# Kernel optimization log

Hardware: AMD Instinct MI355X
Metric: run time of the kernel (lower is better)

Reference implementation:

```python
import jax, jax.numpy as jnp
import numpy as np

BATCH = 32
NUM_VARS = 16
SAMPLES = 4096
EMBED_DIM = 128
WINDOW_SIZE = 32
STEP_SIZE = 4
WIDTH = 1.0


def setup_inputs() -> dict:
    key = jax.random.key(0)
    k1, k2, k3, k4, k5 = jax.random.split(key, 5)
    x = jax.random.normal(k1, (BATCH, NUM_VARS, SAMPLES), dtype=jnp.float32)
    # sample-level LSH: num_variables -> embed_dim
    W_sample = jax.random.normal(k2, (NUM_VARS, EMBED_DIM), dtype=jnp.float32)
    b_sample = jax.random.uniform(k3, (EMBED_DIM,), dtype=jnp.float32, minval=0.0, maxval=WIDTH)
    # patch-level LSH: window_size*embed_dim -> embed_dim
    W_patch = jax.random.normal(k4, (WINDOW_SIZE * EMBED_DIM, EMBED_DIM), dtype=jnp.float32)
    b_patch = jax.random.uniform(k5, (EMBED_DIM,), dtype=jnp.float32, minval=0.0, maxval=WIDTH)
    return {"x": x, "W_sample": W_sample, "b_sample": b_sample,
            "W_patch": W_patch, "b_patch": b_patch}


def reference(x, W_sample, b_sample, W_patch, b_patch):
    batch, v, samples = x.shape
    # encode: E2LSH hash of every timestep, fully vectorized over the samples axis
    # enc: [B, S, D]
    enc = jnp.floor((jnp.einsum('bvs,vd->bsd', x, W_sample) + b_sample) / WIDTH)
    # quantize: sliding windows over time, flattened then hashed
    num_tokens = (samples - WINDOW_SIZE) // STEP_SIZE  # matches preallocated tokens
    # idx: [T, W] gather indices for all windows at once
    idx = jnp.arange(num_tokens)[:, None] * STEP_SIZE + jnp.arange(WINDOW_SIZE)[None, :]
    windows = enc[:, idx, :].reshape(batch, num_tokens, WINDOW_SIZE * EMBED_DIM)  # [B, T, W*D]
    tokens = jnp.floor((windows @ W_patch + b_patch) / WIDTH)  # [B, T, D]
    return tokens
```

## Files before the change

### kernel.cpp

```cpp
#include <hip/hip_runtime.h>
#include <hip/hip_bf16.h>
#include <cstdint>

#define BATCH   32
#define NVARS   16
#define SAMPLES 4096
#define EDIM    128
#define NTOK    1016
#define PLELEM  4368

typedef __bf16 bf8_t __attribute__((ext_vector_type(8)));
typedef float  f4_t  __attribute__((ext_vector_type(4)));

__global__ __launch_bounds__(256) void prep_kernel(
    const float* __restrict__ Wp, __hip_bfloat16* __restrict__ WtF)
{
  __shared__ float ls[32][132];
  int tid = threadIdx.x;
  int kb  = blockIdx.x;
  int s = kb >> 3, dlt = kb & 7;
  int kbase = (4 * dlt + (s & 3)) * 128 + (s >> 2) * 32;
#pragma unroll
  for (int r = 0; r < 16; ++r) {
    int idx = tid + r * 256;
    ls[idx >> 7][idx & 127] =
        Wp[(size_t)(kbase + (idx >> 7)) * EDIM + (idx & 127)];
  }
  __syncthreads();
  int g = tid >> 5, l5 = tid & 31;
#pragma unroll
  for (int h = 0; h < 2; ++h) {
    int lane = l5 + h * 32;
    int quad = lane >> 4, l15 = lane & 15;
    int n = g * 16 + l15;
    union { unsigned short u[8]; uint4 v; } pk;
#pragma unroll
    for (int t = 0; t < 8; ++t) {
      __hip_bfloat16 hh = __float2bfloat16(ls[quad * 8 + t][n]);
      pk.u[t] = *(unsigned short*)&hh;
    }
    *(uint4*)(WtF + (size_t)kb * 4096 + g * 512 + lane * 8) = pk.v;
  }
}

__global__ __launch_bounds__(512, 1) void fused_kernel(
    const float* __restrict__ x,
    const float* __restrict__ Ws,
    const float* __restrict__ bs,
    const __hip_bfloat16* __restrict__ WtF,
    const float* __restrict__ bp,
    float* __restrict__ out)
{
  __shared__ __align__(16) __hip_bfloat16 Apan[16 * PLELEM];
  __shared__ __align__(16) float xTp[2][136][16];

  int tid  = threadIdx.x;
  int lane = tid & 63;
  int wv   = tid >> 6;
  int g    = wv >> 2;
  int wq   = wv & 3;
  int b    = blockIdx.x >> 3;
  int t0   = (blockIdx.x & 7) << 7;
  int wm   = (wq >> 1) << 6;
  int wn   = (wq & 1) << 6;
  int quad = lane >> 4;
  int l15  = lane & 15;

  const __hip_bfloat16* bg = WtF + (size_t)(wn >> 4) * 512 + lane * 8;

  int q4 = tid & 31;
  int eq = q4 >> 3;
  int cq = (q4 >> 1) & 3;
  int hq = q4 & 1;
  int r0 = tid >> 5;

  float w[NVARS][4];
  float bz[4];
  {
    int d0 = q4 * 4;
#pragma unroll
    for (int v = 0; v < NVARS; ++v)
      *(float4*)&w[v][0] = *(const float4*)(Ws + v * EDIM + d0);
    *(float4*)&bz[0] = *(const float4*)(bs + d0);
  }

  int vv = tid & 15, rr = tid >> 4;
  float4 xreg[5];
  {
    const float* xb = x + ((size_t)b * NVARS + vv) * SAMPLES;
#pragma unroll
    for (int j = 0; j < 4; ++j) {
      int s4 = (t0 + rr + 32 * j) * 4;
      xreg[j] = *(const float4*)(xb + s4);
    }
    if (tid < 128) {
      int s4 = (t0 + 128 + rr) * 4;
      if (s4 > SAMPLES - 4) s4 = SAMPLES - 4;
      xreg[4] = *(const float4*)(xb + s4);
    }
  }

  auto stageX = [&](int p, int buf) {
#pragma unroll
    for (int j = 0; j < 4; ++j) {
      float c = (p == 0) ? xreg[j].x : (p == 1) ? xreg[j].y
              : (p == 2) ? xreg[j].z : xreg[j].w;
      xTp[buf][rr + 32 * j][vv] = c;
    }
    if (tid < 128) {
      float c = (p == 0) ? xreg[4].x : (p == 1) ? xreg[4].y
              : (p == 2) ? xreg[4].z : xreg[4].w;
      xTp[buf][128 + rr][vv] = c;
    }
  };

  auto encTask = [&](int p, int buf, int r) {
    const float* xr = &xTp[buf][r][0];
    float xv[NVARS];
    *(float4*)&xv[0]  = *(const float4*)(xr + 0);
    *(float4*)&xv[4]  = *(const float4*)(xr + 4);
    *(float4*)&xv[8]  = *(const float4*)(xr + 8);
    *(float4*)&xv[12] = *(const float4*)(xr + 12);
    float a0 = bz[0], a1 = bz[1], a2 = bz[2], a3 = bz[3];
#pragma unroll
    for (int v = 0; v < NVARS; ++v) {
      a0 += xv[v] * w[v][0]; a1 += xv[v] * w[v][1];
      a2 += xv[v] * w[v][2]; a3 += xv[v] * w[v][3];
    }
    union { unsigned short us[4]; uint2 q; } pk;
    pk.us[0] = (unsigned short)(__float_as_uint(floorf(a0)) >> 16);
    pk.us[1] = (unsigned short)(__float_as_uint(floorf(a1)) >> 16);
    pk.us[2] = (unsigned short)(__float_as_uint(floorf(a2)) >> 16);
    pk.us[3] = (unsigned short)(__float_as_uint(floorf(a3)) >> 16);
    int phys = (cq + (r >> 1)) & 3;
    char* plbase = (char*)&Apan[(eq * 4 + p) * PLELEM];
    *(uint2*)(plbase + r * 64 + phys * 16 + hq * 8) = pk.q;
  };

  stageX(0, 0);
  __syncthreads();
#pragma unroll
  for (int p = 0; p < 4; ++p) {
    if (p < 3) stageX(p + 1, (p + 1) & 1);
    int buf = p & 1;
#pragma unroll
    for (int j = 0; j < 8; ++j) encTask(p, buf, r0 + 16 * j);
    if (tid < 256) encTask(p, buf, 128 + (tid >> 5));
    __syncthreads();
  }

  f4_t acc[4][4];
  f4_t zero = {0.f, 0.f, 0.f, 0.f};
#pragma unroll
  for (int i = 0; i < 4; ++i)
#pragma unroll
    for (int j = 0; j < 4; ++j) acc[i][j] = zero;

  auto loadB = [&](int kb, uint4* d) {
#pragma unroll
    for (int j = 0; j < 4; ++j)
      d[j] = *(const uint4*)(bg + (size_t)kb * 4096 + j * 512);
  };

  auto compute = [&](const bf8_t* pA, int dlt, const uint4* bq_) {
    int swzA = (quad + ((t0 + dlt + wm + l15) >> 1)) & 3;
    bf8_t af[4];
#pragma unroll
    for (int i = 0; i < 4; ++i)
      af[i] = pA[(dlt + wm + i * 16 + l15) * 4 + swzA];
    __builtin_amdgcn_s_setprio(1);
#pragma unroll
    for (int mi = 0; mi < 4; ++mi)
#pragma unroll
      for (int ni = 0; ni < 4; ++ni)
        acc[mi][ni] = __builtin_amdgcn_mfma_f32_16x16x32_bf16(
            af[mi], __builtin_bit_cast(bf8_t, bq_[ni]), acc[mi][ni], 0, 0, 0);
    __builtin_amdgcn_s_setprio(0);
  };

  uint4 bq[2][4];
  loadB(g * 64, bq[0]);
  loadB(g * 64 + 1, bq[1]);

  for (int ss = 0; ss < 8; ++ss) {
    int pl = (g * 2 + (ss >> 2)) * 4 + (ss & 3);
    const bf8_t* pA = (const bf8_t*)&Apan[pl * PLELEM];
#pragma unroll
    for (int d = 0; d < 8; ++d) {
      int kl = ss * 8 + d;
      compute(pA, d, bq[d & 1]);
      if (kl < 62) loadB(g * 64 + kl + 2, bq[d & 1]);
    }
  }

  float* rb = (float*)&Apan[0];
  int widx = (wq * 64 + lane) * 17;
  float bias[4];
#pragma unroll
  for (int ni = 0; ni < 4; ++ni) bias[ni] = bp[wn + ni * 16 + l15];

#pragma unroll
  for (int mi = 0; mi < 4; ++mi) {
    __syncthreads();
    if (g == 1) {
#pragma unroll
      for (int ni = 0; ni < 4; ++ni)
#pragma unroll
        for (int r = 0; r < 4; ++r)
          rb[widx + ni * 4 + r] = acc[mi][ni][r];
    }
    __syncthreads();
    if (g == 0) {
#pragma unroll
      for (int ni = 0; ni < 4; ++ni)
#pragma unroll
        for (int r = 0; r < 4; ++r) {
          int t = t0 + wm + mi * 16 + quad * 4 + r;
          if (t < NTOK) {
            int n = wn + ni * 16 + l15;
            out[((size_t)b * NTOK + t) * EDIM + n] =
                floorf(acc[mi][ni][r] + rb[widx + ni * 4 + r] + bias[ni]);
          }
        }
    }
  }
}

extern "C" void kernel_launch(void* const* d_in, const int* in_sizes, int n_in,
                              void* d_out, int out_size, void* d_ws, size_t ws_size,
                              hipStream_t stream) {
  const float* x  = (const float*)d_in[0];
  const float* Ws = (const float*)d_in[1];
  const float* bs = (const float*)d_in[2];
  const float* Wp = (const float*)d_in[3];
  const float* bp = (const float*)d_in[4];
  float* out = (float*)d_out;

  __hip_bfloat16* WtF = (__hip_bfloat16*)d_ws;

  prep_kernel<<<128, 256, 0, stream>>>(Wp, WtF);
  fused_kernel<<<BATCH * 8, 512, 0, stream>>>(x, Ws, bs, WtF, bp, out);
}
```

Baseline: 106.7 us.

## Split K across four wave groups with full-M tiles and double-buffered A fragments

Each wave now computes all 128 token rows for a 64-column half, and four wave groups split the K dimension instead of two. This halves B-fragment loads per MFMA. A-fragment LDS reads are double-buffered ahead of the MFMAs. The reduction epilogue now sums three partial accumulators through LDS in four rounds. The launch bound asks for 2 blocks per CU while doubling accumulator registers, which risks spills or register pressure, and the LDS footprint may still limit occupancy to one block.

```diff
diff --git a/kernel.cpp b/kernel.cpp
--- a/kernel.cpp
+++ b/kernel.cpp
@@ -43,7 +43,7 @@
   }
 }
 
-__global__ __launch_bounds__(512, 1) void fused_kernel(
+__global__ __launch_bounds__(512, 2) void fused_kernel(
     const float* __restrict__ x,
     const float* __restrict__ Ws,
     const float* __restrict__ bs,
@@ -57,16 +57,14 @@
   int tid  = threadIdx.x;
   int lane = tid & 63;
   int wv   = tid >> 6;
-  int g    = wv >> 2;
-  int wq   = wv & 3;
+  int g2   = wv >> 1;
+  int nh   = wv & 1;
   int b    = blockIdx.x >> 3;
   int t0   = (blockIdx.x & 7) << 7;
-  int wm   = (wq >> 1) << 6;
-  int wn   = (wq & 1) << 6;
   int quad = lane >> 4;
   int l15  = lane & 15;
 
-  const __hip_bfloat16* bg = WtF + (size_t)(wn >> 4) * 512 + lane * 8;
+  const __hip_bfloat16* bg = WtF + (size_t)(nh * 4) * 512 + lane * 8;
 
   int q4 = tid & 31;
   int eq = q4 >> 3;
@@ -149,10 +147,10 @@
     __syncthreads();
   }
 
-  f4_t acc[4][4];
+  f4_t acc[8][4];
   f4_t zero = {0.f, 0.f, 0.f, 0.f};
 #pragma unroll
-  for (int i = 0; i < 4; ++i)
+  for (int i = 0; i < 8; ++i)
 #pragma unroll
     for (int j = 0; j < 4; ++j) acc[i][j] = zero;
 
@@ -162,15 +160,17 @@
       d[j] = *(const uint4*)(bg + (size_t)kb * 4096 + j * 512);
   };
 
-  auto compute = [&](const bf8_t* pA, int dlt, const uint4* bq_) {
-    int swzA = (quad + ((t0 + dlt + wm + l15) >> 1)) & 3;
-    bf8_t af[4];
-#pragma unroll
-    for (int i = 0; i < 4; ++i)
-      af[i] = pA[(dlt + wm + i * 16 + l15) * 4 + swzA];
+  auto loadAF = [&](bf8_t* af, const bf8_t* pA, int dlt) {
+    int swz = (quad + ((t0 + dlt + l15) >> 1)) & 3;
+#pragma unroll
+    for (int i = 0; i < 8; ++i)
+      af[i] = pA[(dlt + i * 16 + l15) * 4 + swz];
+  };
+
+  auto mstep = [&](const bf8_t* af, const uint4* bq_) {
     __builtin_amdgcn_s_setprio(1);
 #pragma unroll
-    for (int mi = 0; mi < 4; ++mi)
+    for (int mi = 0; mi < 8; ++mi)
 #pragma unroll
       for (int ni = 0; ni < 4; ++ni)
         acc[mi][ni] = __builtin_amdgcn_mfma_f32_16x16x32_bf16(
@@ -178,50 +178,76 @@
     __builtin_amdgcn_s_setprio(0);
   };
 
+  bf8_t afA[8], afB[8];
   uint4 bq[2][4];
-  loadB(g * 64, bq[0]);
-  loadB(g * 64 + 1, bq[1]);
-
-  for (int ss = 0; ss < 8; ++ss) {
-    int pl = (g * 2 + (ss >> 2)) * 4 + (ss & 3);
-    const bf8_t* pA = (const bf8_t*)&Apan[pl * PLELEM];
+  loadB(g2 * 32 + 0, bq[0]);
+  loadB(g2 * 32 + 1, bq[1]);
+  loadAF(afA, (const bf8_t*)&Apan[(g2 * 4) * PLELEM], 0);
+
+  for (int ss = 0; ss < 4; ++ss) {
+    const bf8_t* pA  = (const bf8_t*)&Apan[(g2 * 4 + ss) * PLELEM];
+    const bf8_t* pAn = (const bf8_t*)&Apan[(g2 * 4 + ss + 1) * PLELEM];
 #pragma unroll
     for (int d = 0; d < 8; ++d) {
       int kl = ss * 8 + d;
-      compute(pA, d, bq[d & 1]);
-      if (kl < 62) loadB(g * 64 + kl + 2, bq[d & 1]);
-    }
-  }
-
-  float* rb = (float*)&Apan[0];
-  int widx = (wq * 64 + lane) * 17;
+      if ((d & 1) == 0) {
+        if (d < 7) loadAF(afB, pA, d + 1);
+        mstep(afA, bq[0]);
+      } else {
+        if (d < 7)      loadAF(afA, pA, d + 1);
+        else if (ss < 3) loadAF(afA, pAn, 0);
+        mstep(afB, bq[1]);
+      }
+      if (kl < 30) loadB(g2 * 32 + kl + 2, bq[d & 1]);
+    }
+  }
+
+  float* rb2 = (float*)&Apan[0];
   float bias[4];
 #pragma unroll
-  for (int ni = 0; ni < 4; ++ni) bias[ni] = bp[wn + ni * 16 + l15];
-
-#pragma unroll
-  for (int mi = 0; mi < 4; ++mi) {
+  for (int ni = 0; ni < 4; ++ni) bias[ni] = bp[(nh << 6) + ni * 16 + l15];
+
+#pragma unroll
+  for (int rd = 0; rd < 4; ++rd) {
     __syncthreads();
-    if (g == 1) {
-#pragma unroll
-      for (int ni = 0; ni < 4; ++ni)
-#pragma unroll
-        for (int r = 0; r < 4; ++r)
-          rb[widx + ni * 4 + r] = acc[mi][ni][r];
+    if (g2 > 0) {
+      int slot = ((g2 - 1) * 2 + nh) * 64 + lane;
+#pragma unroll
+      for (int mh = 0; mh < 2; ++mh) {
+        int mi = rd * 2 + mh;
+#pragma unroll
+        for (int ni = 0; ni < 4; ++ni)
+          *(f4_t*)&rb2[(size_t)(slot + mh * 384) * 20 + ni * 4] = acc[mi][ni];
+      }
     }
     __syncthreads();
-    if (g == 0) {
-#pragma unroll
-      for (int ni = 0; ni < 4; ++ni)
-#pragma unroll
-        for (int r = 0; r < 4; ++r) {
-          int t = t0 + wm + mi * 16 + quad * 4 + r;
-          if (t < NTOK) {
-            int n = wn + ni * 16 + l15;
-            out[((size_t)b * NTOK + t) * EDIM + n] =
-                floorf(acc[mi][ni][r] + rb[widx + ni * 4 + r] + bias[ni]);
+    if (g2 == 0) {
+#pragma unroll
+      for (int mh = 0; mh < 2; ++mh) {
+        int mi = rd * 2 + mh;
+        f4_t s0 = acc[mi][0], s1 = acc[mi][1];
+        f4_t s2 = acc[mi][2], s3 = acc[mi][3];
+#pragma unroll
+        for (int q = 1; q < 4; ++q) {
+          int sl = ((q - 1) * 2 + nh) * 64 + lane + mh * 384;
+          s0 += *(const f4_t*)&rb2[(size_t)sl * 20 + 0];
+          s1 += *(const f4_t*)&rb2[(size_t)sl * 20 + 4];
+          s2 += *(const f4_t*)&rb2[(size_t)sl * 20 + 8];
+          s3 += *(const f4_t*)&rb2[(size_t)sl * 20 + 12];
+        }
+        f4_t sv[4] = {s0, s1, s2, s3};
+#pragma unroll
+        for (int ni = 0; ni < 4; ++ni)
+#pragma unroll
+          for (int r = 0; r < 4; ++r) {
+            int t = t0 + mi * 16 + quad * 4 + r;
+            if (t < NTOK) {
+              int n = (nh << 6) + ni * 16 + l15;
+              out[((size_t)b * NTOK + t) * EDIM + n] =
+                  floorf(sv[ni][r] + bias[ni]);
+            }
           }
-        }
+      }
     }
   }
 }
```

Result: slower. 110.5 us (+3.5%).
